# Kernel tuning notes

Measured on AMD Instinct MI355X. Metric: run time of the kernel, lower is better.

Reference implementation:

```python
import jax, jax.numpy as jnp
import numpy as np

N_NODES = 50000
N_EDGES = 600000
N_GRAPHS = 64
IN_D, HID, EMB = 5, 128, 64
BN_EPS = 1e-5


def setup_inputs() -> dict:
    key = jax.random.key(0)
    ks = jax.random.split(key, 16)
    x = jax.random.normal(ks[0], (N_NODES, IN_D), dtype=jnp.float32)
    src = jax.random.randint(ks[1], (N_EDGES,), 0, N_NODES, dtype=jnp.int32)
    dst = jax.random.randint(ks[2], (N_EDGES,), 0, N_NODES, dtype=jnp.int32)
    batch = jnp.sort(jax.random.randint(ks[3], (N_NODES,), 0, N_GRAPHS, dtype=jnp.int32))
    def lin(k, fi, fo):
        s = 1.0 / np.sqrt(fi)
        kw, kb = jax.random.split(k)
        return (jax.random.uniform(kw, (fi, fo), jnp.float32, -s, s),
                jax.random.uniform(kb, (fo,), jnp.float32, -s, s))
    W1, b1 = lin(ks[4], IN_D, HID)
    W2, b2 = lin(ks[5], HID, HID)
    W3, b3 = lin(ks[6], HID, HID)
    Wp, bp = lin(ks[7], HID, EMB)
    g1 = 1.0 + 0.1 * jax.random.normal(ks[8], (HID,), jnp.float32)
    g2 = 1.0 + 0.1 * jax.random.normal(ks[9], (HID,), jnp.float32)
    g3 = 1.0 + 0.1 * jax.random.normal(ks[10], (HID,), jnp.float32)
    be1 = 0.1 * jax.random.normal(ks[11], (HID,), jnp.float32)
    be2 = 0.1 * jax.random.normal(ks[12], (HID,), jnp.float32)
    be3 = 0.1 * jax.random.normal(ks[13], (HID,), jnp.float32)
    return dict(x=x, src=src, dst=dst, batch=batch,
                W1=W1, b1=b1, W2=W2, b2=b2, W3=W3, b3=b3,
                g1=g1, be1=be1, g2=g2, be2=be2, g3=g3, be3=be3,
                Wp=Wp, bp=bp)


def reference(x, src, dst, batch, W1, b1, W2, b2, W3, b3,
              g1, be1, g2, be2, g3, be3, Wp, bp):
    n = x.shape[0]
    # GCNConv with self-loops and symmetric normalization (PyG default)
    loop = jnp.arange(n, dtype=src.dtype)
    s = jnp.concatenate([src, loop])
    d = jnp.concatenate([dst, loop])
    deg = jax.ops.segment_sum(jnp.ones_like(d, dtype=x.dtype), d, num_segments=n)
    dinv = jnp.where(deg > 0, jax.lax.rsqrt(deg), 0.0)
    norm = (dinv[s] * dinv[d])[:, None]  # (E+N, 1)

    def gcn(h, W, b):
        hw = h @ W                                   # (N, HID)
        msg = hw[s] * norm                           # gather + scale
        agg = jax.ops.segment_sum(msg, d, num_segments=n)
        return agg + b

    def bn_relu(h, g, be):
        # eval-mode BatchNorm1d with running_mean=0, running_var=1
        return jax.nn.relu(h * (g * jax.lax.rsqrt(jnp.asarray(1.0 + BN_EPS, h.dtype))) + be)

    h = bn_relu(gcn(x, W1, b1), g1, be1)
    h = bn_relu(gcn(h, W2, b2), g2, be2)
    h = bn_relu(gcn(h, W3, b3), g3, be3)

    # global mean pool over graphs
    sums = jax.ops.segment_sum(h, batch, num_segments=N_GRAPHS)
    cnt = jax.ops.segment_sum(jnp.ones((n,), h.dtype), batch, num_segments=N_GRAPHS)
    pooled = sums / jnp.maximum(cnt, 1.0)[:, None]
    return pooled @ Wp + bp
```

## Files before the change

kernel.cpp:

```cpp
#include <hip/hip_runtime.h>
#include <hip/hip_fp16.h>

#define N_NODES 50000
#define N_EDGES 600000
#define N_GRAPHS 64
#define IN_D 5
#define HID 128
#define EMB 64

#define CHUNK 512
#define NCHUNK ((N_NODES + CHUNK - 1) / CHUNK)
#define NREP 16
#define NLOC 4
#define TB 16

typedef _Float16 half8 __attribute__((ext_vector_type(8)));
typedef float float4v __attribute__((ext_vector_type(4)));


__global__ __launch_bounds__(256) void k_init(
        int* __restrict__ cnt, float* __restrict__ psum_rep,
        const float* __restrict__ W2, const float* __restrict__ W3,
        _Float16* __restrict__ Wt2, _Float16* __restrict__ Wt3) {
    int tid = blockIdx.x * blockDim.x + threadIdx.x;
    int nt = gridDim.x * blockDim.x;
    for (int i = tid; i < N_NODES; i += nt) cnt[i] = 0;
    for (int i = tid; i < NREP * N_GRAPHS * HID; i += nt) psum_rep[i] = 0.f;
    for (int i = tid; i < 2 * HID * HID; i += nt) {
        int rem = i & (HID * HID - 1);
        int k = rem & 127, f = rem >> 7;
        if (i < HID * HID) Wt2[rem] = (_Float16)W2[k * HID + f];
        else               Wt3[rem] = (_Float16)W3[k * HID + f];
    }
}


__global__ __launch_bounds__(256) void k_count(
        const int* __restrict__ dst, int* __restrict__ cnt) {
    int e = blockIdx.x * blockDim.x + threadIdx.x;
    if (e < N_EDGES) atomicAdd(&cnt[dst[e]], 1);
}


__global__ void k_chunksum(const int* __restrict__ cnt, int* __restrict__ csum,
                           float* __restrict__ dinv) {
    __shared__ int sh[256];
    int b = blockIdx.x, t = threadIdx.x;
    int i0 = b * CHUNK + t, i1 = i0 + 256;
    int v = 0;
    if (i0 < N_NODES) { int c = cnt[i0]; v += c; dinv[i0] = rsqrtf((float)c + 1.0f); }
    if (i1 < N_NODES) { int c = cnt[i1]; v += c; dinv[i1] = rsqrtf((float)c + 1.0f); }
    sh[t] = v; __syncthreads();
    for (int off = 128; off > 0; off >>= 1) {
        if (t < off) sh[t] += sh[t + off];
        __syncthreads();
    }
    if (t == 0) csum[b] = sh[0];
}


__global__ void k_scan(const int* __restrict__ cnt, const int* __restrict__ csum,
                       int* __restrict__ row_start) {
    __shared__ int ws[4];
    int b = blockIdx.x, t = threadIdx.x;
    int lane = t & 63, w = t >> 6;

    int pre = 0;
    for (int j = lane; j < b; j += 64) pre += csum[j];
    #pragma unroll
    for (int off = 32; off > 0; off >>= 1) pre += __shfl_down(pre, off);
    pre = __shfl(pre, 0);

    int base = b * CHUNK;
    int i0 = base + 2 * t, i1 = i0 + 1;
    int c0 = (i0 < N_NODES) ? cnt[i0] : 0;
    int c1 = (i1 < N_NODES) ? cnt[i1] : 0;
    int v = c0 + c1;
    int s = v;
    #pragma unroll
    for (int off = 1; off < 64; off <<= 1) {
        int u = __shfl_up(s, off);
        if (lane >= off) s += u;
    }
    if (lane == 63) ws[w] = s;
    __syncthreads();
    if (t == 0) {
        int r = 0;
        #pragma unroll
        for (int j = 0; j < 4; ++j) { int xx = ws[j]; ws[j] = r; r += xx; }
    }
    __syncthreads();
    int excl = s - v + ws[w] + pre;
    if (i0 < N_NODES) row_start[i0] = excl;
    if (i1 < N_NODES) row_start[i1] = excl + c0;
    if (b == 0 && t == 0) row_start[N_NODES] = N_EDGES;
}


__global__ __launch_bounds__(256) void k_scatter(
        const int* __restrict__ src, const int* __restrict__ dst,
        const float* __restrict__ dinv, const int* __restrict__ row_start,
        int* __restrict__ cnt, int2* __restrict__ e_pack) {
    int e = blockIdx.x * blockDim.x + threadIdx.x;
    if (e >= N_EDGES) return;
    int d = dst[e];
    int pos = row_start[d] + atomicSub(&cnt[d], 1) - 1;
    int s = src[e];
    e_pack[pos] = make_int2(s, __float_as_int(dinv[s]));
}


__global__ __launch_bounds__(256) void k_agg5g1(
        const float* __restrict__ x, const float* __restrict__ dinv,
        const int* __restrict__ row_start, const int2* __restrict__ e_pack,
        const float* __restrict__ W1, const float* __restrict__ b1,
        const float* __restrict__ g1, const float* __restrict__ be1,
        __half2* __restrict__ H16) {
    int gid = blockIdx.x * blockDim.x + threadIdx.x;
    int i = gid >> 3, k = gid & 7;
    if (i >= N_NODES) return;
    float acc = 0.f;
    if (k < IN_D) {
        int beg = row_start[i], end = row_start[i + 1];
        int e = beg;
        for (; e + 3 < end; e += 4) {
            int2 p0 = e_pack[e];
            int2 p1 = e_pack[e + 1];
            int2 p2 = e_pack[e + 2];
            int2 p3 = e_pack[e + 3];
            float x0 = x[p0.x * IN_D + k];
            float x1 = x[p1.x * IN_D + k];
            float x2 = x[p2.x * IN_D + k];
            float x3 = x[p3.x * IN_D + k];
            acc = fmaf(__int_as_float(p0.y), x0, acc);
            acc = fmaf(__int_as_float(p1.y), x1, acc);
            acc = fmaf(__int_as_float(p2.y), x2, acc);
            acc = fmaf(__int_as_float(p3.y), x3, acc);
        }
        for (; e < end; ++e) {
            int2 p = e_pack[e];
            acc = fmaf(__int_as_float(p.y), x[p.x * IN_D + k], acc);
        }
        float di = dinv[i];
        acc = di * (acc + di * x[i * IN_D + k]);
    }
    int lane = threadIdx.x & 63;
    int base = lane & ~7;
    float a0 = __shfl(acc, base + 0);
    float a1 = __shfl(acc, base + 1);
    float a2 = __shfl(acc, base + 2);
    float a3 = __shfl(acc, base + 3);
    float a4 = __shfl(acc, base + 4);
    const float rs = rsqrtf(1.0f + 1e-5f);
    int f0 = k * 16;
    #pragma unroll
    for (int u = 0; u < 8; ++u) {
        int fa = f0 + u * 2, fb = fa + 1;
        float va = b1[fa], vb = b1[fb];
        va = fmaf(a0, W1[0 * HID + fa], va); vb = fmaf(a0, W1[0 * HID + fb], vb);
        va = fmaf(a1, W1[1 * HID + fa], va); vb = fmaf(a1, W1[1 * HID + fb], vb);
        va = fmaf(a2, W1[2 * HID + fa], va); vb = fmaf(a2, W1[2 * HID + fb], vb);
        va = fmaf(a3, W1[3 * HID + fa], va); vb = fmaf(a3, W1[3 * HID + fb], vb);
        va = fmaf(a4, W1[4 * HID + fa], va); vb = fmaf(a4, W1[4 * HID + fb], vb);
        va = fmaf(va, g1[fa] * rs, be1[fa]);
        vb = fmaf(vb, g1[fb] * rs, be1[fb]);
        va = va > 0.f ? va : 0.f;
        vb = vb > 0.f ? vb : 0.f;
        H16[(size_t)i * 64 + k * 8 + u] = __floats2half2_rn(va, vb);
    }
}


__device__ __forceinline__ float2 agg_node(
        const __half2* __restrict__ Hin, const float* __restrict__ dinv,
        const int* __restrict__ row_start, const int2* __restrict__ e_pack,
        int n, int lane) {
    float2 acc = make_float2(0.f, 0.f);
    int beg = row_start[n], end = row_start[n + 1];
    int e = beg;
    for (; e + 7 < end; e += 8) {
        int2 p[8];
        __half2 rh[8];
        #pragma unroll
        for (int u = 0; u < 8; ++u) p[u] = e_pack[e + u];
        #pragma unroll
        for (int u = 0; u < 8; ++u) rh[u] = Hin[(size_t)p[u].x * 64 + lane];
        #pragma unroll
        for (int u = 0; u < 8; ++u) {
            float w = __int_as_float(p[u].y);
            float2 f = __half22float2(rh[u]);
            acc.x = fmaf(w, f.x, acc.x);
            acc.y = fmaf(w, f.y, acc.y);
        }
    }
    for (; e + 3 < end; e += 4) {
        int2 p[4];
        __half2 rh[4];
        #pragma unroll
        for (int u = 0; u < 4; ++u) p[u] = e_pack[e + u];
        #pragma unroll
        for (int u = 0; u < 4; ++u) rh[u] = Hin[(size_t)p[u].x * 64 + lane];
        #pragma unroll
        for (int u = 0; u < 4; ++u) {
            float w = __int_as_float(p[u].y);
            float2 f = __half22float2(rh[u]);
            acc.x = fmaf(w, f.x, acc.x);
            acc.y = fmaf(w, f.y, acc.y);
        }
    }
    for (; e < end; ++e) {
        int2 pe = e_pack[e];
        float w = __int_as_float(pe.y);
        float2 f = __half22float2(Hin[(size_t)pe.x * 64 + lane]);
        acc.x = fmaf(w, f.x, acc.x);
        acc.y = fmaf(w, f.y, acc.y);
    }
    float di = dinv[n];
    float2 hs = __half22float2(Hin[(size_t)n * 64 + lane]);
    acc.x = di * fmaf(di, hs.x, acc.x);
    acc.y = di * fmaf(di, hs.y, acc.y);
    return acc;
}


__global__ __launch_bounds__(256) void k_fuse2(
        const __half2* __restrict__ Hin, const float* __restrict__ dinv,
        const int* __restrict__ row_start, const int2* __restrict__ e_pack,
        const _Float16* __restrict__ Wt,
        const float* __restrict__ bb, const float* __restrict__ gg,
        const float* __restrict__ bee, _Float16* __restrict__ outH) {
    __shared__ __align__(16) _Float16 As[TB][136];
    int t = threadIdx.x;
    int w = t >> 6, lane = t & 63;
    int nb = blockIdx.x * TB;

    #pragma unroll 1
    for (int i = 0; i < 4; ++i) {
        int n = nb + w * 4 + i;
        float2 r = agg_node(Hin, dinv, row_start, e_pack, n, lane);
        *(__half2*)&As[w * 4 + i][2 * lane] = __floats2half2_rn(r.x, r.y);
    }
    __syncthreads();

    int quad = lane >> 4, r16 = lane & 15;
    half8 a[4];
    #pragma unroll
    for (int kb = 0; kb < 4; ++kb)
        a[kb] = *(const half8*)&As[r16][(kb * 4 + quad) * 8];
    const float rs = rsqrtf(1.0f + 1e-5f);
    #pragma unroll
    for (int fi = 0; fi < 2; ++fi) {
        int f = (w * 2 + fi) * 16 + r16;
        const half8* Brow = (const half8*)(Wt + (size_t)f * 128);
        float4v acc = {0.f, 0.f, 0.f, 0.f};
        #pragma unroll
        for (int kb = 0; kb < 4; ++kb)
            acc = __builtin_amdgcn_mfma_f32_16x16x32_f16(a[kb], Brow[kb * 4 + quad],
                                                         acc, 0, 0, 0);
        float b0 = bb[f], gf = gg[f] * rs, e0 = bee[f];
        #pragma unroll
        for (int rr = 0; rr < 4; ++rr) {
            float v = fmaf(acc[rr] + b0, gf, e0);
            v = v > 0.f ? v : 0.f;
            outH[(size_t)(nb + quad * 4 + rr) * 128 + f] = (_Float16)v;
        }
    }
}


__global__ __launch_bounds__(256) void k_fuse3(
        const __half2* __restrict__ Hin, const float* __restrict__ dinv,
        const int* __restrict__ row_start, const int2* __restrict__ e_pack,
        const _Float16* __restrict__ Wt,
        const float* __restrict__ bb, const float* __restrict__ gg,
        const float* __restrict__ bee, const int* __restrict__ batch,
        float* __restrict__ psum_rep) {
    __shared__ __align__(16) _Float16 As[TB][136];
    __shared__ float sh_pool[NLOC][HID];
    int t = threadIdx.x;
    int w = t >> 6, lane = t & 63;
    int blk = (int)blockIdx.x;
    int nb = blk * TB;

    for (int i = t; i < NLOC * HID; i += 256) ((float*)sh_pool)[i] = 0.f;

    #pragma unroll 1
    for (int i = 0; i < 4; ++i) {
        int n = nb + w * 4 + i;
        float2 r = agg_node(Hin, dinv, row_start, e_pack, n, lane);
        *(__half2*)&As[w * 4 + i][2 * lane] = __floats2half2_rn(r.x, r.y);
    }
    int quad = lane >> 4, r16 = lane & 15;
    int g0 = batch[nb];
    int gi4[4];
    #pragma unroll
    for (int rr = 0; rr < 4; ++rr) gi4[rr] = batch[nb + quad * 4 + rr];
    __syncthreads();

    half8 a[4];
    #pragma unroll
    for (int kb = 0; kb < 4; ++kb)
        a[kb] = *(const half8*)&As[r16][(kb * 4 + quad) * 8];
    float* rep = psum_rep + (size_t)(blk & (NREP - 1)) * N_GRAPHS * HID;
    const float rs = rsqrtf(1.0f + 1e-5f);
    #pragma unroll
    for (int fi = 0; fi < 2; ++fi) {
        int f = (w * 2 + fi) * 16 + r16;
        const half8* Brow = (const half8*)(Wt + (size_t)f * 128);
        float4v acc = {0.f, 0.f, 0.f, 0.f};
        #pragma unroll
        for (int kb = 0; kb < 4; ++kb)
            acc = __builtin_amdgcn_mfma_f32_16x16x32_f16(a[kb], Brow[kb * 4 + quad],
                                                         acc, 0, 0, 0);
        float b0 = bb[f], gf = gg[f] * rs, e0 = bee[f];
        float partial = 0.f;
        int cur = -1;
        #pragma unroll
        for (int rr = 0; rr < 4; ++rr) {
            float v = fmaf(acc[rr] + b0, gf, e0);
            v = v > 0.f ? v : 0.f;
            int gi = gi4[rr];
            if (gi != cur) {
                if (cur >= 0) {
                    int idx = cur - g0;
                    if (idx < NLOC) atomicAdd(&sh_pool[idx][f], partial);
                    else            atomicAdd(&rep[cur * HID + f], partial);
                }
                partial = 0.f; cur = gi;
            }
            partial += v;
        }
        if (cur >= 0) {
            int idx = cur - g0;
            if (idx < NLOC) atomicAdd(&sh_pool[idx][f], partial);
            else            atomicAdd(&rep[cur * HID + f], partial);
        }
    }
    __syncthreads();
    for (int i = t; i < NLOC * HID; i += 256) {
        int idx = i >> 7, f = i & 127;
        float v = sh_pool[idx][f];
        int g = g0 + idx;
        if (v != 0.f && g < N_GRAPHS) atomicAdd(&rep[g * HID + f], v);
    }
}


__device__ __forceinline__ int lower_bound_batch(const int* __restrict__ batch, int val) {
    int lo = 0, hi = N_NODES;
    while (lo < hi) {
        int mid = (lo + hi) >> 1;
        if (batch[mid] < val) lo = mid + 1;
        else hi = mid;
    }
    return lo;
}

__global__ void k_final(const float* __restrict__ psum_rep, const int* __restrict__ batch,
                        const float* __restrict__ Wp, const float* __restrict__ bp,
                        float* __restrict__ out) {
    __shared__ float s_p[HID];
    int gi = blockIdx.x, e = threadIdx.x;
    for (int f = e; f < HID; f += EMB) {
        float v = 0.f;
        #pragma unroll
        for (int r = 0; r < NREP; ++r)
            v += psum_rep[(size_t)r * N_GRAPHS * HID + gi * HID + f];
        s_p[f] = v;
    }
    int lane = e & 63;
    int r = 0;
    if (lane < 2) r = lower_bound_batch(batch, gi + lane);
    int c0 = __shfl(r, 0), c1 = __shfl(r, 1);
    float inv = 1.0f / fmaxf((float)(c1 - c0), 1.0f);
    __syncthreads();
    float acc = bp[e];
    #pragma unroll 8
    for (int f = 0; f < HID; ++f)
        acc = fmaf(s_p[f] * inv, Wp[f * EMB + e], acc);
    out[gi * EMB + e] = acc;
}


extern "C" void kernel_launch(void* const* d_in, const int* in_sizes, int n_in,
                              void* d_out, int out_size, void* d_ws, size_t ws_size,
                              hipStream_t stream) {
    const float* x   = (const float*)d_in[0];
    const int*   src = (const int*)d_in[1];
    const int*   dst = (const int*)d_in[2];
    const int* batch = (const int*)d_in[3];
    const float* W1 = (const float*)d_in[4];
    const float* b1 = (const float*)d_in[5];
    const float* W2 = (const float*)d_in[6];
    const float* b2 = (const float*)d_in[7];
    const float* W3 = (const float*)d_in[8];
    const float* b3 = (const float*)d_in[9];
    const float* g1 = (const float*)d_in[10];
    const float* be1 = (const float*)d_in[11];
    const float* g2 = (const float*)d_in[12];
    const float* be2 = (const float*)d_in[13];
    const float* g3 = (const float*)d_in[14];
    const float* be3 = (const float*)d_in[15];
    const float* Wp = (const float*)d_in[16];
    const float* bp = (const float*)d_in[17];
    float* out = (float*)d_out;

    char* ws = (char*)d_ws;
    size_t o = 0;
    auto alloc = [&](size_t bytes) {
        void* pp = ws + o;
        o += bytes;
        o = (o + 255) & ~255ull;
        return pp;
    };
    int*      cnt       = (int*)alloc(N_NODES * 4);
    int*      row_start = (int*)alloc((N_NODES + 1) * 4);
    int*      csum      = (int*)alloc(NCHUNK * 4);
    float*    dinv      = (float*)alloc(N_NODES * 4);
    int2*     e_pack    = (int2*)alloc((size_t)N_EDGES * 8);
    _Float16* Wt2       = (_Float16*)alloc(HID * HID * 2);
    _Float16* Wt3       = (_Float16*)alloc(HID * HID * 2);
    __half2*  H16       = (__half2*)alloc((size_t)(N_NODES + 64) * HID * 2);
    __half2*  A16       = (__half2*)alloc((size_t)(N_NODES + 64) * HID * 2);
    float*    psum_rep  = (float*)alloc((size_t)NREP * N_GRAPHS * HID * 4);

    k_init<<<512, 256, 0, stream>>>(cnt, psum_rep, W2, W3, Wt2, Wt3);
    k_count<<<(N_EDGES + 255) / 256, 256, 0, stream>>>(dst, cnt);
    k_chunksum<<<NCHUNK, 256, 0, stream>>>(cnt, csum, dinv);
    k_scan<<<NCHUNK, 256, 0, stream>>>(cnt, csum, row_start);
    k_scatter<<<(N_EDGES + 255) / 256, 256, 0, stream>>>(src, dst, dinv, row_start,
                                                         cnt, e_pack);
    k_agg5g1<<<(N_NODES * 8 + 255) / 256, 256, 0, stream>>>(x, dinv, row_start, e_pack,
                                                            W1, b1, g1, be1, H16);
    k_fuse2<<<N_NODES / TB, 256, 0, stream>>>(H16, dinv, row_start, e_pack, Wt2,
                                              b2, g2, be2, (_Float16*)A16);
    k_fuse3<<<N_NODES / TB, 256, 0, stream>>>((const __half2*)A16, dinv, row_start,
                                              e_pack, Wt3, b3, g3, be3, batch, psum_rep);
    k_final<<<N_GRAPHS, EMB, 0, stream>>>(psum_rep, batch, Wp, bp, out);
}
```

Before: 274.9 us.

## Balance edge aggregation across warps per tile using flat edge ranges and LDS atomics

Replaces per-node aggregation (each wavefront handling 4 fixed nodes) with a scheme where the 16-node tile's edge range is split evenly across the 4 wavefronts. Each wavefront walks its contiguous edge slice and flushes partial sums into an fp32 LDS tile with atomics at node boundaries. It also software-pipelines the edge-index loads, and the self-loop term and the destination dinv scaling are applied later. The aim is to remove load imbalance from skewed degrees, at the cost of LDS atomics, fp32 staging and extra branching. It also adds an occupancy hint to the launch bounds.

```diff
diff --git a/kernel.cpp b/kernel.cpp
--- a/kernel.cpp
+++ b/kernel.cpp
@@ -13,6 +13,7 @@
 #define NREP 16
 #define NLOC 4
 #define TB 16
+#define ASTRIDE 132
 
 typedef _Float16 half8 __attribute__((ext_vector_type(8)));
 typedef float float4v __attribute__((ext_vector_type(4)));
@@ -171,82 +172,113 @@
 }
 
 
-__device__ __forceinline__ float2 agg_node(
+__device__ __forceinline__ void agg_tile_edges(
         const __half2* __restrict__ Hin, const float* __restrict__ dinv,
-        const int* __restrict__ row_start, const int2* __restrict__ e_pack,
-        int n, int lane) {
-    float2 acc = make_float2(0.f, 0.f);
-    int beg = row_start[n], end = row_start[n + 1];
-    int e = beg;
-    for (; e + 7 < end; e += 8) {
-        int2 p[8];
-        __half2 rh[8];
-        #pragma unroll
-        for (int u = 0; u < 8; ++u) p[u] = e_pack[e + u];
-        #pragma unroll
-        for (int u = 0; u < 8; ++u) rh[u] = Hin[(size_t)p[u].x * 64 + lane];
+        const int2* __restrict__ e_pack, const int* __restrict__ rs_s,
+        float* __restrict__ AsF, int nb, int w, int lane) {
+    int E0 = rs_s[0], E1 = rs_s[16];
+    int Etot = E1 - E0;
+    int per = (Etot + 3) >> 2;
+    int s0 = E0 + w * per;
+    int s1 = s0 + per; if (s1 > E1) s1 = E1;
+
+    if (s0 < s1) {
+        int j = 0;
+        while (rs_s[j + 1] <= s0) ++j;
+        int rsNext = rs_s[j + 1];
+        float2 acc = make_float2(0.f, 0.f);
+        int2 P0[8], P1[8];
         #pragma unroll
         for (int u = 0; u < 8; ++u) {
-            float w = __int_as_float(p[u].y);
-            float2 f = __half22float2(rh[u]);
-            acc.x = fmaf(w, f.x, acc.x);
-            acc.y = fmaf(w, f.y, acc.y);
-        }
-    }
-    for (; e + 3 < end; e += 4) {
-        int2 p[4];
-        __half2 rh[4];
-        #pragma unroll
-        for (int u = 0; u < 4; ++u) p[u] = e_pack[e + u];
-        #pragma unroll
-        for (int u = 0; u < 4; ++u) rh[u] = Hin[(size_t)p[u].x * 64 + lane];
-        #pragma unroll
-        for (int u = 0; u < 4; ++u) {
-            float w = __int_as_float(p[u].y);
-            float2 f = __half22float2(rh[u]);
-            acc.x = fmaf(w, f.x, acc.x);
-            acc.y = fmaf(w, f.y, acc.y);
-        }
-    }
-    for (; e < end; ++e) {
-        int2 pe = e_pack[e];
-        float w = __int_as_float(pe.y);
-        float2 f = __half22float2(Hin[(size_t)pe.x * 64 + lane]);
-        acc.x = fmaf(w, f.x, acc.x);
-        acc.y = fmaf(w, f.y, acc.y);
-    }
-    float di = dinv[n];
-    float2 hs = __half22float2(Hin[(size_t)n * 64 + lane]);
-    acc.x = di * fmaf(di, hs.x, acc.x);
-    acc.y = di * fmaf(di, hs.y, acc.y);
-    return acc;
-}
-
-
-__global__ __launch_bounds__(256) void k_fuse2(
+            int idx = s0 + u;
+            P0[u] = e_pack[idx < E1 ? idx : E1 - 1];
+        }
+        int e = s0;
+        while (e < s1) {
+            #pragma unroll
+            for (int u = 0; u < 8; ++u) {
+                int idx = e + 8 + u;
+                P1[u] = e_pack[idx < E1 ? idx : E1 - 1];
+            }
+            __half2 G[8];
+            #pragma unroll
+            for (int u = 0; u < 8; ++u)
+                G[u] = Hin[(size_t)P0[u].x * 64 + lane];
+            #pragma unroll
+            for (int u = 0; u < 8; ++u) {
+                if (e + u < s1) {
+                    while (e + u >= rsNext) {
+                        if (acc.x != 0.f || acc.y != 0.f) {
+                            atomicAdd(&AsF[j * ASTRIDE + 2 * lane], acc.x);
+                            atomicAdd(&AsF[j * ASTRIDE + 2 * lane + 1], acc.y);
+                        }
+                        acc = make_float2(0.f, 0.f);
+                        ++j; rsNext = rs_s[j + 1];
+                    }
+                    float wgt = __int_as_float(P0[u].y);
+                    float2 f = __half22float2(G[u]);
+                    acc.x = fmaf(wgt, f.x, acc.x);
+                    acc.y = fmaf(wgt, f.y, acc.y);
+                }
+            }
+            #pragma unroll
+            for (int u = 0; u < 8; ++u) P0[u] = P1[u];
+            e += 8;
+        }
+        if (acc.x != 0.f || acc.y != 0.f) {
+            atomicAdd(&AsF[j * ASTRIDE + 2 * lane], acc.x);
+            atomicAdd(&AsF[j * ASTRIDE + 2 * lane + 1], acc.y);
+        }
+    }
+    {
+        int jl = w * 4;
+        __half2 S[4]; float dv[4];
+        #pragma unroll
+        for (int i2 = 0; i2 < 4; ++i2) {
+            int n = nb + jl + i2;
+            S[i2] = Hin[(size_t)n * 64 + lane];
+            dv[i2] = dinv[n];
+        }
+        #pragma unroll
+        for (int i2 = 0; i2 < 4; ++i2) {
+            float2 f = __half22float2(S[i2]);
+            atomicAdd(&AsF[(jl + i2) * ASTRIDE + 2 * lane], dv[i2] * f.x);
+            atomicAdd(&AsF[(jl + i2) * ASTRIDE + 2 * lane + 1], dv[i2] * f.y);
+        }
+    }
+}
+
+
+__global__ __launch_bounds__(256, 4) void k_fuse2(
         const __half2* __restrict__ Hin, const float* __restrict__ dinv,
         const int* __restrict__ row_start, const int2* __restrict__ e_pack,
         const _Float16* __restrict__ Wt,
         const float* __restrict__ bb, const float* __restrict__ gg,
         const float* __restrict__ bee, _Float16* __restrict__ outH) {
-    __shared__ __align__(16) _Float16 As[TB][136];
+    __shared__ __align__(16) float AsF[TB * ASTRIDE];
+    __shared__ int rs_s[TB + 1];
     int t = threadIdx.x;
     int w = t >> 6, lane = t & 63;
     int nb = blockIdx.x * TB;
 
-    #pragma unroll 1
-    for (int i = 0; i < 4; ++i) {
-        int n = nb + w * 4 + i;
-        float2 r = agg_node(Hin, dinv, row_start, e_pack, n, lane);
-        *(__half2*)&As[w * 4 + i][2 * lane] = __floats2half2_rn(r.x, r.y);
-    }
+    if (t < TB + 1) rs_s[t] = row_start[nb + t];
+    for (int i = t; i < TB * ASTRIDE; i += 256) AsF[i] = 0.f;
+    __syncthreads();
+
+    agg_tile_edges(Hin, dinv, e_pack, rs_s, AsF, nb, w, lane);
     __syncthreads();
 
     int quad = lane >> 4, r16 = lane & 15;
+    float dv = dinv[nb + r16];
     half8 a[4];
     #pragma unroll
-    for (int kb = 0; kb < 4; ++kb)
-        a[kb] = *(const half8*)&As[r16][(kb * 4 + quad) * 8];
+    for (int kb = 0; kb < 4; ++kb) {
+        const float* srcp = &AsF[r16 * ASTRIDE + (kb * 4 + quad) * 8];
+        half8 h;
+        #pragma unroll
+        for (int q2 = 0; q2 < 8; ++q2) h[q2] = (_Float16)(dv * srcp[q2]);
+        a[kb] = h;
+    }
     const float rs = rsqrtf(1.0f + 1e-5f);
     #pragma unroll
     for (int fi = 0; fi < 2; ++fi) {
@@ -268,39 +300,45 @@
 }
 
 
-__global__ __launch_bounds__(256) void k_fuse3(
+__global__ __launch_bounds__(256, 4) void k_fuse3(
         const __half2* __restrict__ Hin, const float* __restrict__ dinv,
         const int* __restrict__ row_start, const int2* __restrict__ e_pack,
         const _Float16* __restrict__ Wt,
         const float* __restrict__ bb, const float* __restrict__ gg,
         const float* __restrict__ bee, const int* __restrict__ batch,
         float* __restrict__ psum_rep) {
-    __shared__ __align__(16) _Float16 As[TB][136];
+    __shared__ __align__(16) float AsF[TB * ASTRIDE];
+    __shared__ int rs_s[TB + 1];
     __shared__ float sh_pool[NLOC][HID];
     int t = threadIdx.x;
     int w = t >> 6, lane = t & 63;
     int blk = (int)blockIdx.x;
     int nb = blk * TB;
 
+    if (t < TB + 1) rs_s[t] = row_start[nb + t];
+    for (int i = t; i < TB * ASTRIDE; i += 256) AsF[i] = 0.f;
     for (int i = t; i < NLOC * HID; i += 256) ((float*)sh_pool)[i] = 0.f;
-
-    #pragma unroll 1
-    for (int i = 0; i < 4; ++i) {
-        int n = nb + w * 4 + i;
-        float2 r = agg_node(Hin, dinv, row_start, e_pack, n, lane);
-        *(__half2*)&As[w * 4 + i][2 * lane] = __floats2half2_rn(r.x, r.y);
-    }
+    __syncthreads();
+
+    agg_tile_edges(Hin, dinv, e_pack, rs_s, AsF, nb, w, lane);
+    __syncthreads();
+
     int quad = lane >> 4, r16 = lane & 15;
+    float dv = dinv[nb + r16];
+    half8 a[4];
+    #pragma unroll
+    for (int kb = 0; kb < 4; ++kb) {
+        const float* srcp = &AsF[r16 * ASTRIDE + (kb * 4 + quad) * 8];
+        half8 h;
+        #pragma unroll
+        for (int q2 = 0; q2 < 8; ++q2) h[q2] = (_Float16)(dv * srcp[q2]);
+        a[kb] = h;
+    }
     int g0 = batch[nb];
     int gi4[4];
     #pragma unroll
     for (int rr = 0; rr < 4; ++rr) gi4[rr] = batch[nb + quad * 4 + rr];
-    __syncthreads();
-
-    half8 a[4];
-    #pragma unroll
-    for (int kb = 0; kb < 4; ++kb)
-        a[kb] = *(const half8*)&As[r16][(kb * 4 + quad) * 8];
+
     float* rep = psum_rep + (size_t)(blk & (NREP - 1)) * N_GRAPHS * HID;
     const float rs = rsqrtf(1.0f + 1e-5f);
     #pragma unroll
```

Measured after the change: 361.5 us. +31.5%, slower.

## Split each wavefront into four edge slots with 16-byte feature gathers

Applied to the files above, without the earlier changes.

Changes per-node neighbour aggregation so that a 64-lane wavefront handles four edges at once. Each 16-lane group loads a full 128-feature fp16 row using 16-byte vector loads, and the partial sums are combined with cross-lane shuffles. This is meant to cut the number of memory instructions and raise memory-level parallelism per gather compared to the old approach, which read one half2 per lane per edge. The trade-offs are masked-lane waste on low-degree nodes, extra shuffle work, and padding the edge array so tail reads stay in bounds.

```diff
diff --git a/kernel.cpp b/kernel.cpp
--- a/kernel.cpp
+++ b/kernel.cpp
@@ -21,11 +21,13 @@
 __global__ __launch_bounds__(256) void k_init(
         int* __restrict__ cnt, float* __restrict__ psum_rep,
         const float* __restrict__ W2, const float* __restrict__ W3,
-        _Float16* __restrict__ Wt2, _Float16* __restrict__ Wt3) {
+        _Float16* __restrict__ Wt2, _Float16* __restrict__ Wt3,
+        int2* __restrict__ e_pack) {
     int tid = blockIdx.x * blockDim.x + threadIdx.x;
     int nt = gridDim.x * blockDim.x;
     for (int i = tid; i < N_NODES; i += nt) cnt[i] = 0;
     for (int i = tid; i < NREP * N_GRAPHS * HID; i += nt) psum_rep[i] = 0.f;
+    if (tid < 8) e_pack[N_EDGES + tid] = make_int2(0, 0);
     for (int i = tid; i < 2 * HID * HID; i += nt) {
         int rem = i & (HID * HID - 1);
         int k = rem & 127, f = rem >> 7;
@@ -171,60 +173,46 @@
 }
 
 
-__device__ __forceinline__ float2 agg_node(
-        const __half2* __restrict__ Hin, const float* __restrict__ dinv,
+__device__ __forceinline__ void agg_node_mf(
+        const _Float16* __restrict__ Hin, const float* __restrict__ dinv,
         const int* __restrict__ row_start, const int2* __restrict__ e_pack,
-        int n, int lane) {
-    float2 acc = make_float2(0.f, 0.f);
+        int n, int slot, int q16, _Float16* __restrict__ asrow) {
+    float acc[8];
+    #pragma unroll
+    for (int j = 0; j < 8; ++j) acc[j] = 0.f;
     int beg = row_start[n], end = row_start[n + 1];
-    int e = beg;
-    for (; e + 7 < end; e += 8) {
-        int2 p[8];
-        __half2 rh[8];
-        #pragma unroll
-        for (int u = 0; u < 8; ++u) p[u] = e_pack[e + u];
-        #pragma unroll
-        for (int u = 0; u < 8; ++u) rh[u] = Hin[(size_t)p[u].x * 64 + lane];
-        #pragma unroll
-        for (int u = 0; u < 8; ++u) {
-            float w = __int_as_float(p[u].y);
-            float2 f = __half22float2(rh[u]);
-            acc.x = fmaf(w, f.x, acc.x);
-            acc.y = fmaf(w, f.y, acc.y);
-        }
-    }
-    for (; e + 3 < end; e += 4) {
-        int2 p[4];
-        __half2 rh[4];
-        #pragma unroll
-        for (int u = 0; u < 4; ++u) p[u] = e_pack[e + u];
-        #pragma unroll
-        for (int u = 0; u < 4; ++u) rh[u] = Hin[(size_t)p[u].x * 64 + lane];
-        #pragma unroll
-        for (int u = 0; u < 4; ++u) {
-            float w = __int_as_float(p[u].y);
-            float2 f = __half22float2(rh[u]);
-            acc.x = fmaf(w, f.x, acc.x);
-            acc.y = fmaf(w, f.y, acc.y);
-        }
-    }
-    for (; e < end; ++e) {
-        int2 pe = e_pack[e];
-        float w = __int_as_float(pe.y);
-        float2 f = __half22float2(Hin[(size_t)pe.x * 64 + lane]);
-        acc.x = fmaf(w, f.x, acc.x);
-        acc.y = fmaf(w, f.y, acc.y);
+    for (int e = beg; e < end; e += 8) {
+        int2 peA = e_pack[e + slot];
+        float fwA = (e + slot < end) ? __int_as_float(peA.y) : 0.f;
+        half8 gA = ((const half8*)(Hin + (size_t)peA.x * HID))[q16];
+        #pragma unroll
+        for (int j = 0; j < 8; ++j) acc[j] = fmaf(fwA, (float)gA[j], acc[j]);
+        if (e + 4 < end) {
+            int2 peB = e_pack[e + 4 + slot];
+            float fwB = (e + 4 + slot < end) ? __int_as_float(peB.y) : 0.f;
+            half8 gB = ((const half8*)(Hin + (size_t)peB.x * HID))[q16];
+            #pragma unroll
+            for (int j = 0; j < 8; ++j) acc[j] = fmaf(fwB, (float)gB[j], acc[j]);
+        }
+    }
+    #pragma unroll
+    for (int j = 0; j < 8; ++j) {
+        acc[j] += __shfl_xor(acc[j], 16);
+        acc[j] += __shfl_xor(acc[j], 32);
     }
     float di = dinv[n];
-    float2 hs = __half22float2(Hin[(size_t)n * 64 + lane]);
-    acc.x = di * fmaf(di, hs.x, acc.x);
-    acc.y = di * fmaf(di, hs.y, acc.y);
-    return acc;
+    half8 hs = ((const half8*)(Hin + (size_t)n * HID))[q16];
+    half8 outv;
+    #pragma unroll
+    for (int j = 0; j < 8; ++j)
+        outv[j] = (_Float16)(di * fmaf(di, (float)hs[j], acc[j]));
+    if (slot == 0)
+        *(half8*)(asrow + q16 * 8) = outv;
 }
 
 
 __global__ __launch_bounds__(256) void k_fuse2(
-        const __half2* __restrict__ Hin, const float* __restrict__ dinv,
+        const _Float16* __restrict__ Hin, const float* __restrict__ dinv,
         const int* __restrict__ row_start, const int2* __restrict__ e_pack,
         const _Float16* __restrict__ Wt,
         const float* __restrict__ bb, const float* __restrict__ gg,
@@ -232,14 +220,13 @@
     __shared__ __align__(16) _Float16 As[TB][136];
     int t = threadIdx.x;
     int w = t >> 6, lane = t & 63;
+    int slot = lane >> 4, q16 = lane & 15;
     int nb = blockIdx.x * TB;
 
     #pragma unroll 1
-    for (int i = 0; i < 4; ++i) {
-        int n = nb + w * 4 + i;
-        float2 r = agg_node(Hin, dinv, row_start, e_pack, n, lane);
-        *(__half2*)&As[w * 4 + i][2 * lane] = __floats2half2_rn(r.x, r.y);
-    }
+    for (int i = 0; i < 4; ++i)
+        agg_node_mf(Hin, dinv, row_start, e_pack, nb + w * 4 + i,
+                    slot, q16, &As[w * 4 + i][0]);
     __syncthreads();
 
     int quad = lane >> 4, r16 = lane & 15;
@@ -269,7 +256,7 @@
 
 
 __global__ __launch_bounds__(256) void k_fuse3(
-        const __half2* __restrict__ Hin, const float* __restrict__ dinv,
+        const _Float16* __restrict__ Hin, const float* __restrict__ dinv,
         const int* __restrict__ row_start, const int2* __restrict__ e_pack,
         const _Float16* __restrict__ Wt,
         const float* __restrict__ bb, const float* __restrict__ gg,
@@ -279,17 +266,17 @@
     __shared__ float sh_pool[NLOC][HID];
     int t = threadIdx.x;
     int w = t >> 6, lane = t & 63;
+    int slot = lane >> 4, q16 = lane & 15;
     int blk = (int)blockIdx.x;
     int nb = blk * TB;
 
     for (int i = t; i < NLOC * HID; i += 256) ((float*)sh_pool)[i] = 0.f;
 
     #pragma unroll 1
-    for (int i = 0; i < 4; ++i) {
-        int n = nb + w * 4 + i;
-        float2 r = agg_node(Hin, dinv, row_start, e_pack, n, lane);
-        *(__half2*)&As[w * 4 + i][2 * lane] = __floats2half2_rn(r.x, r.y);
-    }
+    for (int i = 0; i < 4; ++i)
+        agg_node_mf(Hin, dinv, row_start, e_pack, nb + w * 4 + i,
+                    slot, q16, &As[w * 4 + i][0]);
+
     int quad = lane >> 4, r16 = lane & 15;
     int g0 = batch[nb];
     int gi4[4];
@@ -338,10 +325,10 @@
     }
     __syncthreads();
     for (int i = t; i < NLOC * HID; i += 256) {
-        int idx = i >> 7, f = i & 127;
-        float v = sh_pool[idx][f];
+        int idx = i >> 7, ff = i & 127;
+        float v = sh_pool[idx][ff];
         int g = g0 + idx;
-        if (v != 0.f && g < N_GRAPHS) atomicAdd(&rep[g * HID + f], v);
+        if (v != 0.f && g < N_GRAPHS) atomicAdd(&rep[g * HID + ff], v);
     }
 }
 
@@ -417,14 +404,14 @@
     int*      row_start = (int*)alloc((N_NODES + 1) * 4);
     int*      csum      = (int*)alloc(NCHUNK * 4);
     float*    dinv      = (float*)alloc(N_NODES * 4);
-    int2*     e_pack    = (int2*)alloc((size_t)N_EDGES * 8);
+    int2*     e_pack    = (int2*)alloc((size_t)(N_EDGES + 8) * 8);
     _Float16* Wt2       = (_Float16*)alloc(HID * HID * 2);
     _Float16* Wt3       = (_Float16*)alloc(HID * HID * 2);
     __half2*  H16       = (__half2*)alloc((size_t)(N_NODES + 64) * HID * 2);
     __half2*  A16       = (__half2*)alloc((size_t)(N_NODES + 64) * HID * 2);
     float*    psum_rep  = (float*)alloc((size_t)NREP * N_GRAPHS * HID * 4);
 
-    k_init<<<512, 256, 0, stream>>>(cnt, psum_rep, W2, W3, Wt2, Wt3);
+    k_init<<<512, 256, 0, stream>>>(cnt, psum_rep, W2, W3, Wt2, Wt3, e_pack);
     k_count<<<(N_EDGES + 255) / 256, 256, 0, stream>>>(dst, cnt);
     k_chunksum<<<NCHUNK, 256, 0, stream>>>(cnt, csum, dinv);
     k_scan<<<NCHUNK, 256, 0, stream>>>(cnt, csum, row_start);
@@ -432,9 +419,9 @@
                                                          cnt, e_pack);
     k_agg5g1<<<(N_NODES * 8 + 255) / 256, 256, 0, stream>>>(x, dinv, row_start, e_pack,
                                                             W1, b1, g1, be1, H16);
-    k_fuse2<<<N_NODES / TB, 256, 0, stream>>>(H16, dinv, row_start, e_pack, Wt2,
-                                              b2, g2, be2, (_Float16*)A16);
-    k_fuse3<<<N_NODES / TB, 256, 0, stream>>>((const __half2*)A16, dinv, row_start,
+    k_fuse2<<<N_NODES / TB, 256, 0, stream>>>((const _Float16*)H16, dinv, row_start,
+                                              e_pack, Wt2, b2, g2, be2, (_Float16*)A16);
+    k_fuse3<<<N_NODES / TB, 256, 0, stream>>>((const _Float16*)A16, dinv, row_start,
                                               e_pack, Wt3, b3, g3, be3, batch, psum_rep);
     k_final<<<N_GRAPHS, EMB, 0, stream>>>(psum_rep, batch, Wp, bp, out);
 }
```

Measured after the change: 280.5 us. 2.1% more time.
